# Optimization experiments

Measured on AMD Instinct MI355X. Metric: run time of the kernel, lower is better.

The kernel has to match this reference:

```python
import jax, jax.numpy as jnp
import numpy as np

N_NODES = 100000
N_EDGES = 1600000
IN_DIM = 128
OUT_DIM = 128
LEAKY_SLOPE = 0.01  # torch nn.LeakyReLU default


def setup_inputs() -> dict:
    key = jax.random.key(0)
    k1, k2, k3, k4 = jax.random.split(key, 4)
    x = jax.random.normal(k1, (N_NODES, IN_DIM), dtype=jnp.float32)
    edge_index = jax.random.randint(k2, (2, N_EDGES), 0, N_NODES, dtype=jnp.int64)
    edge_attr = jax.random.uniform(k3, (N_EDGES,), dtype=jnp.float32)
    # Linear params (xavier_uniform weight, zero bias)
    limit = np.sqrt(6.0 / (IN_DIM + OUT_DIM)).astype(np.float32)
    W = jax.random.uniform(k4, (OUT_DIM, IN_DIM), minval=-limit, maxval=limit, dtype=jnp.float32)
    b = jnp.zeros((OUT_DIM,), dtype=jnp.float32)
    return {"x": x, "edge_index": edge_index, "edge_attr": edge_attr, "W": W, "b": b}


def reference(x, edge_index, edge_attr, W, b):
    src = edge_index[0]  # x_j (source nodes)
    dst = edge_index[1]  # aggregation index (target nodes)
    # message: gather source features, scale by per-edge scalar  [E, D]
    msg = x[src] * edge_attr[:, None]
    # aggregate: scatter-add over target index  [N, D]
    agg = jax.ops.segment_sum(msg, dst, num_segments=N_NODES)
    # update: Linear + LeakyReLU (dropout is identity at p=0 / eval)
    out = agg @ W.T + b
    return jnp.where(out >= 0, out, LEAKY_SLOPE * out)
```

## Files before the change

kernel.cpp:

```cpp
#include <hip/hip_runtime.h>

#define N_NODES 100000
#define N_EDGES 1600000
#define DIM 128
#define LEAKY 0.01f
#define RS_STRIDE 132
#define WS_STRIDE 132
#define NBUCKET 391
#define SB_EDGES 4096
#define NSB 391

typedef short bf16x8 __attribute__((ext_vector_type(8)));
typedef float f32x4 __attribute__((ext_vector_type(4)));

static __device__ __forceinline__ unsigned short f2bf(float f) {
  unsigned int u = __float_as_uint(f);
  u = (u + 0x7fffu + ((u >> 16) & 1u)) >> 16;
  return (unsigned short)u;
}

__global__ __launch_bounds__(512) void sort_local_kernel(
    const int* __restrict__ ei, const float* __restrict__ attr,
    int2* __restrict__ binned, unsigned short* __restrict__ counts,
    int* __restrict__ srcOff) {
  __shared__ int hist[NBUCKET];
  __shared__ int cursor[NBUCKET];
  __shared__ int scanBuf[512];
  __shared__ int2 stage[SB_EDGES];

  const int t = threadIdx.x;
  const int blk = blockIdx.x;
  const int base = blk * SB_EDGES;
  const int n = min(SB_EDGES, N_EDGES - base);

  if (t < NBUCKET) hist[t] = 0;
  __syncthreads();

  int myP[8];
  int myB[8];
  float myA[8];
#pragma unroll
  for (int k = 0; k < 8; ++k) {
    int i = t + k * 512;
    if (i < n) {
      int e = base + i;
      int s = ei[e];
      int d = ei[N_EDGES + e];
      myA[k] = attr[e];
      myB[k] = d >> 8;
      myP[k] = s | ((d & 255) << 17);
      atomicAdd(&hist[myB[k]], 1);
    } else {
      myB[k] = -1;
    }
  }
  __syncthreads();

  int v = (t < NBUCKET) ? hist[t] : 0;
  scanBuf[t] = v;
  __syncthreads();
  for (int off = 1; off < 512; off <<= 1) {
    int u = (t >= off) ? scanBuf[t - off] : 0;
    __syncthreads();
    scanBuf[t] += u;
    __syncthreads();
  }
  if (t < NBUCKET) {
    int excl = scanBuf[t] - v;
    cursor[t] = excl;
    counts[(size_t)t * NSB + blk] = (unsigned short)v;
    srcOff[(size_t)t * NSB + blk] = base + excl;
  }
  __syncthreads();

#pragma unroll
  for (int k = 0; k < 8; ++k) {
    if (myB[k] >= 0) {
      int loc = atomicAdd(&cursor[myB[k]], 1);
      stage[loc] = make_int2(myP[k], __float_as_int(myA[k]));
    }
  }
  __syncthreads();

  for (int i = t; i < n; i += 512) binned[base + i] = stage[i];
}

__global__ __launch_bounds__(128) void bucket_count_kernel(
    const unsigned short* __restrict__ counts, int* __restrict__ bucketCount) {
  __shared__ int red[128];
  const int b = blockIdx.x;
  const int t = threadIdx.x;
  int s = 0;
  for (int sb = t; sb < NSB; sb += 128) s += counts[(size_t)b * NSB + sb];
  red[t] = s;
  __syncthreads();
  for (int off = 64; off > 0; off >>= 1) {
    if (t < off) red[t] += red[t + off];
    __syncthreads();
  }
  if (t == 0) bucketCount[b] = red[0];
}

__global__ __launch_bounds__(512) void bucket_scan_kernel(
    const int* __restrict__ bucketCount, int* __restrict__ bucketBase) {
  __shared__ int s[512];
  const int t = threadIdx.x;
  int v = (t < NBUCKET) ? bucketCount[t] : 0;
  s[t] = v;
  __syncthreads();
  for (int off = 1; off < 512; off <<= 1) {
    int u = (t >= off) ? s[t - off] : 0;
    __syncthreads();
    s[t] += u;
    __syncthreads();
  }
  if (t < NBUCKET) bucketBase[t] = s[t] - v;
}

__global__ __launch_bounds__(448) void passB_kernel(
    const int2* __restrict__ binned, const unsigned short* __restrict__ counts,
    const int* __restrict__ srcOff, const int* __restrict__ bucketBase,
    int2* __restrict__ csr, int* __restrict__ row_ptr) {
  __shared__ int runSrc[NSB];
  __shared__ int runLen[NSB];
  __shared__ int hist[256];
  __shared__ int cur[256];
  __shared__ int scanBuf[256];

  const int b = blockIdx.x;
  const int t = threadIdx.x;

  if (t < NSB) {
    runSrc[t] = srcOff[(size_t)b * NSB + t];
    runLen[t] = (int)counts[(size_t)b * NSB + t];
  }
  if (t < 256) hist[t] = 0;
  __syncthreads();

  if (t < NSB) {
    const int src = runSrc[t];
    const int len = runLen[t];
    for (int j = 0; j < len; ++j) {
      int px = binned[src + j].x;
      atomicAdd(&hist[(px >> 17) & 255], 1);
    }
  }
  __syncthreads();

  int hv = (t < 256) ? hist[t] : 0;
  if (t < 256) scanBuf[t] = hv;
  __syncthreads();
  for (int off = 1; off < 256; off <<= 1) {
    int u = 0;
    if (t < 256 && t >= off) u = scanBuf[t - off];
    __syncthreads();
    if (t < 256) scanBuf[t] += u;
    __syncthreads();
  }
  const int bb = bucketBase[b];
  if (t < 256) {
    int excl = scanBuf[t] - hv;
    cur[t] = excl;
    int node = b * 256 + t;
    if (node < N_NODES) row_ptr[node] = bb + excl;
  }
  if (b == 0 && t == 0) row_ptr[N_NODES] = N_EDGES;
  __syncthreads();

  if (t < NSB) {
    const int src = runSrc[t];
    const int len = runLen[t];
    for (int j = 0; j < len; ++j) {
      int2 rec = binned[src + j];
      int ld = (rec.x >> 17) & 255;
      int pos = bb + atomicAdd(&cur[ld], 1);
      csr[pos] = make_int2(rec.x & 0x1FFFF, rec.y);
    }
  }
}

__global__ __launch_bounds__(256) void x2b_kernel(
    const float4* __restrict__ x, ushort4* __restrict__ xb) {
  const int i = blockIdx.x * 256 + threadIdx.x;
  float4 v = x[i];
  ushort4 o;
  o.x = f2bf(v.x); o.y = f2bf(v.y); o.z = f2bf(v.z); o.w = f2bf(v.w);
  xb[i] = o;
}

__global__ __launch_bounds__(256) void w_frag_kernel(
    const float* __restrict__ W, bf16x8* __restrict__ wfrag) {
  const int gid = blockIdx.x * 256 + threadIdx.x;
  const int lane = gid & 63;
  const int q = (gid >> 6) & 3;
  const int nt = gid >> 8;
  const int n = nt * 16 + (lane & 15);
  const int kb = q * 32 + ((lane >> 4) & 3) * 8;
  const float4 f0 = *(const float4*)(W + n * DIM + kb);
  const float4 f1 = *(const float4*)(W + n * DIM + kb + 4);
  bf16x8 frag;
  frag[0] = (short)f2bf(f0.x); frag[1] = (short)f2bf(f0.y);
  frag[2] = (short)f2bf(f0.z); frag[3] = (short)f2bf(f0.w);
  frag[4] = (short)f2bf(f1.x); frag[5] = (short)f2bf(f1.y);
  frag[6] = (short)f2bf(f1.z); frag[7] = (short)f2bf(f1.w);
  wfrag[gid] = frag;
}

__global__ __launch_bounds__(256) void gather_aggb_kernel(
    const unsigned short* __restrict__ xb, const int* __restrict__ row_ptr,
    const int2* __restrict__ csr, unsigned int* __restrict__ aggB) {
  const int w = threadIdx.x >> 6;
  const int lane = threadIdx.x & 63;
  const int nA = blockIdx.x * 8 + w * 2;
  const int nB = nA + 1;

  int a = row_ptr[nA];
  const int aEnd = row_ptr[nA + 1];
  int b = row_ptr[nB];
  const int bEnd = row_ptr[nB + 1];

  float2 accA = make_float2(0.f, 0.f);
  float2 accB = make_float2(0.f, 0.f);

  while (a + 5 < aEnd && b + 5 < bEnd) {
    int2 ea[6], eb[6];
#pragma unroll
    for (int k = 0; k < 6; ++k) {
      ea[k] = csr[a + k];
      eb[k] = csr[b + k];
    }
    unsigned int ua[6], ub[6];
#pragma unroll
    for (int k = 0; k < 6; ++k) {
      ua[k] = *(const unsigned int*)(xb + (size_t)ea[k].x * DIM + lane * 2);
      ub[k] = *(const unsigned int*)(xb + (size_t)eb[k].x * DIM + lane * 2);
    }
#pragma unroll
    for (int k = 0; k < 6; ++k) {
      float fa = __int_as_float(ea[k].y);
      float fb = __int_as_float(eb[k].y);
      accA.x += __uint_as_float(ua[k] << 16) * fa;
      accA.y += __uint_as_float(ua[k] & 0xffff0000u) * fa;
      accB.x += __uint_as_float(ub[k] << 16) * fb;
      accB.y += __uint_as_float(ub[k] & 0xffff0000u) * fb;
    }
    a += 6;
    b += 6;
  }

  for (; a + 3 < aEnd; a += 4) {
    int2 e[4];
#pragma unroll
    for (int k = 0; k < 4; ++k) e[k] = csr[a + k];
    unsigned int u[4];
#pragma unroll
    for (int k = 0; k < 4; ++k)
      u[k] = *(const unsigned int*)(xb + (size_t)e[k].x * DIM + lane * 2);
#pragma unroll
    for (int k = 0; k < 4; ++k) {
      float f = __int_as_float(e[k].y);
      accA.x += __uint_as_float(u[k] << 16) * f;
      accA.y += __uint_as_float(u[k] & 0xffff0000u) * f;
    }
  }
  for (; a < aEnd; ++a) {
    int2 e0 = csr[a];
    float f0 = __int_as_float(e0.y);
    unsigned int u0 = *(const unsigned int*)(xb + (size_t)e0.x * DIM + lane * 2);
    accA.x += __uint_as_float(u0 << 16) * f0;
    accA.y += __uint_as_float(u0 & 0xffff0000u) * f0;
  }

  for (; b + 3 < bEnd; b += 4) {
    int2 e[4];
#pragma unroll
    for (int k = 0; k < 4; ++k) e[k] = csr[b + k];
    unsigned int u[4];
#pragma unroll
    for (int k = 0; k < 4; ++k)
      u[k] = *(const unsigned int*)(xb + (size_t)e[k].x * DIM + lane * 2);
#pragma unroll
    for (int k = 0; k < 4; ++k) {
      float f = __int_as_float(e[k].y);
      accB.x += __uint_as_float(u[k] << 16) * f;
      accB.y += __uint_as_float(u[k] & 0xffff0000u) * f;
    }
  }
  for (; b < bEnd; ++b) {
    int2 e0 = csr[b];
    float f0 = __int_as_float(e0.y);
    unsigned int u0 = *(const unsigned int*)(xb + (size_t)e0.x * DIM + lane * 2);
    accB.x += __uint_as_float(u0 << 16) * f0;
    accB.y += __uint_as_float(u0 & 0xffff0000u) * f0;
  }

  aggB[(size_t)nA * 64 + lane] =
      (unsigned int)f2bf(accA.x) | ((unsigned int)f2bf(accA.y) << 16);
  aggB[(size_t)nB * 64 + lane] =
      (unsigned int)f2bf(accB.x) | ((unsigned int)f2bf(accB.y) << 16);
}

__global__ __launch_bounds__(256) void gather_bf16_kernel(
    const unsigned short* __restrict__ xb, const int* __restrict__ row_ptr,
    const int2* __restrict__ csr, float* __restrict__ out) {
  const int node = blockIdx.x * 4 + (threadIdx.x >> 6);
  const int lane = threadIdx.x & 63;

  const int beg = row_ptr[node];
  const int end = row_ptr[node + 1];

  float2 acc = make_float2(0.f, 0.f);
  int e = beg;
  for (; e + 3 < end; e += 4) {
    int2 e0 = csr[e];
    int2 e1 = csr[e + 1];
    int2 e2 = csr[e + 2];
    int2 e3 = csr[e + 3];
    unsigned int u0 = *(const unsigned int*)(xb + (size_t)e0.x * DIM + lane * 2);
    unsigned int u1 = *(const unsigned int*)(xb + (size_t)e1.x * DIM + lane * 2);
    unsigned int u2 = *(const unsigned int*)(xb + (size_t)e2.x * DIM + lane * 2);
    unsigned int u3 = *(const unsigned int*)(xb + (size_t)e3.x * DIM + lane * 2);
    float a0 = __int_as_float(e0.y), a1 = __int_as_float(e1.y);
    float a2 = __int_as_float(e2.y), a3 = __int_as_float(e3.y);
    acc.x += __uint_as_float(u0 << 16) * a0;
    acc.y += __uint_as_float(u0 & 0xffff0000u) * a0;
    acc.x += __uint_as_float(u1 << 16) * a1;
    acc.y += __uint_as_float(u1 & 0xffff0000u) * a1;
    acc.x += __uint_as_float(u2 << 16) * a2;
    acc.y += __uint_as_float(u2 & 0xffff0000u) * a2;
    acc.x += __uint_as_float(u3 << 16) * a3;
    acc.y += __uint_as_float(u3 & 0xffff0000u) * a3;
  }
  for (; e < end; ++e) {
    int2 e0 = csr[e];
    float a0 = __int_as_float(e0.y);
    unsigned int u0 = *(const unsigned int*)(xb + (size_t)e0.x * DIM + lane * 2);
    acc.x += __uint_as_float(u0 << 16) * a0;
    acc.y += __uint_as_float(u0 & 0xffff0000u) * a0;
  }
  *(float2*)(out + (size_t)node * DIM + lane * 2) = acc;
}

__global__ __launch_bounds__(256) void gather_f32_kernel(
    const float* __restrict__ x, const int* __restrict__ row_ptr,
    const int2* __restrict__ csr, float* __restrict__ out) {
  const int node = blockIdx.x * 4 + (threadIdx.x >> 6);
  const int lane = threadIdx.x & 63;

  const int beg = row_ptr[node];
  const int end = row_ptr[node + 1];

  float2 acc = make_float2(0.f, 0.f);
  int e = beg;
  for (; e + 3 < end; e += 4) {
    int2 e0 = csr[e];
    int2 e1 = csr[e + 1];
    int2 e2 = csr[e + 2];
    int2 e3 = csr[e + 3];
    float2 v0 = *(const float2*)(x + (size_t)e0.x * DIM + lane * 2);
    float2 v1 = *(const float2*)(x + (size_t)e1.x * DIM + lane * 2);
    float2 v2 = *(const float2*)(x + (size_t)e2.x * DIM + lane * 2);
    float2 v3 = *(const float2*)(x + (size_t)e3.x * DIM + lane * 2);
    float a0 = __int_as_float(e0.y), a1 = __int_as_float(e1.y);
    float a2 = __int_as_float(e2.y), a3 = __int_as_float(e3.y);
    acc.x += v0.x * a0; acc.y += v0.y * a0;
    acc.x += v1.x * a1; acc.y += v1.y * a1;
    acc.x += v2.x * a2; acc.y += v2.y * a2;
    acc.x += v3.x * a3; acc.y += v3.y * a3;
  }
  for (; e < end; ++e) {
    int2 e0 = csr[e];
    float a0 = __int_as_float(e0.y);
    float2 v0 = *(const float2*)(x + (size_t)e0.x * DIM + lane * 2);
    acc.x += v0.x * a0; acc.y += v0.y * a0;
  }
  *(float2*)(out + (size_t)node * DIM + lane * 2) = acc;
}

__global__ __launch_bounds__(256) void linear_mfma_bf16_kernel(
    const unsigned short* __restrict__ aggB, const bf16x8* __restrict__ wfrag,
    const float* __restrict__ bias, float* __restrict__ out) {
  const int wave = threadIdx.x >> 6;
  const int lane = threadIdx.x & 63;
  const int r0 = (blockIdx.x * 4 + wave) * 16;
  if (r0 >= N_NODES) return;

  const int m = lane & 15;
  const int quad = lane >> 4;
  const int row = r0 + m;

  bf16x8 afrag[4];
#pragma unroll
  for (int q = 0; q < 4; ++q) {
    afrag[q] = *(const bf16x8*)(aggB + (size_t)row * DIM + q * 32 + quad * 8);
  }

#pragma unroll
  for (int nt = 0; nt < 8; ++nt) {
    const float bv = bias[nt * 16 + m];
    f32x4 acc = {bv, bv, bv, bv};
#pragma unroll
    for (int q = 0; q < 4; ++q) {
      bf16x8 bfrag = wfrag[(nt * 4 + q) * 64 + lane];
      acc = __builtin_amdgcn_mfma_f32_16x16x32_bf16(afrag[q], bfrag, acc, 0, 0, 0);
    }
    const int col = nt * 16 + m;
#pragma unroll
    for (int i = 0; i < 4; ++i) {
      float v = acc[i];
      v = v >= 0.f ? v : v * LEAKY;
      out[(size_t)(r0 + quad * 4 + i) * DIM + col] = v;
    }
  }
}

__global__ __launch_bounds__(256) void linear_mfma_kernel(
    const float* __restrict__ agg, const bf16x8* __restrict__ wfrag,
    const float* __restrict__ bias, float* __restrict__ out) {
  const int wave = threadIdx.x >> 6;
  const int lane = threadIdx.x & 63;
  const int r0 = (blockIdx.x * 4 + wave) * 16;
  if (r0 >= N_NODES) return;

  const int m = lane & 15;
  const int quad = lane >> 4;
  const int row = r0 + m;

  bf16x8 afrag[4];
#pragma unroll
  for (int q = 0; q < 4; ++q) {
    const float* ap = agg + (size_t)row * DIM + q * 32 + quad * 8;
    const float4 f0 = *(const float4*)(ap);
    const float4 f1 = *(const float4*)(ap + 4);
    afrag[q][0] = (short)f2bf(f0.x); afrag[q][1] = (short)f2bf(f0.y);
    afrag[q][2] = (short)f2bf(f0.z); afrag[q][3] = (short)f2bf(f0.w);
    afrag[q][4] = (short)f2bf(f1.x); afrag[q][5] = (short)f2bf(f1.y);
    afrag[q][6] = (short)f2bf(f1.z); afrag[q][7] = (short)f2bf(f1.w);
  }

#pragma unroll
  for (int nt = 0; nt < 8; ++nt) {
    const float bv = bias[nt * 16 + m];
    f32x4 acc = {bv, bv, bv, bv};
#pragma unroll
    for (int q = 0; q < 4; ++q) {
      bf16x8 bfrag = wfrag[(nt * 4 + q) * 64 + lane];
      acc = __builtin_amdgcn_mfma_f32_16x16x32_bf16(afrag[q], bfrag, acc, 0, 0, 0);
    }
    const int col = nt * 16 + m;
#pragma unroll
    for (int i = 0; i < 4; ++i) {
      float v = acc[i];
      v = v >= 0.f ? v : v * LEAKY;
      out[(size_t)(r0 + quad * 4 + i) * DIM + col] = v;
    }
  }
}

__global__ __launch_bounds__(256) void scatter_kernel(
    const float* __restrict__ x, const int* __restrict__ ei,
    const float* __restrict__ attr, float* __restrict__ agg) {
  int gid = blockIdx.x * blockDim.x + threadIdx.x;
  int e = gid >> 5;
  int f = (gid & 31) * 4;
  if (e >= N_EDGES) return;
  int s = ei[e];
  int d = ei[N_EDGES + e];
  float a = attr[e];
  const float4 xv = *(const float4*)(x + (size_t)s * DIM + f);
  float* dp = agg + (size_t)d * DIM + f;
  atomicAdd(dp + 0, xv.x * a);
  atomicAdd(dp + 1, xv.y * a);
  atomicAdd(dp + 2, xv.z * a);
  atomicAdd(dp + 3, xv.w * a);
}

__global__ __launch_bounds__(256, 2) void linear_kernel(
    const float* __restrict__ agg, const float* __restrict__ W,
    const float* __restrict__ bias, float* __restrict__ out) {
  __shared__ float Rs[32 * RS_STRIDE];
  __shared__ float Ws[64 * WS_STRIDE];

  const int tid = threadIdx.x;
  const int c = (tid & 31) * 4;
  const int rg = tid >> 5;
  const size_t rowBase = (size_t)blockIdx.x * 32;

  {
    const int lr = tid >> 3;
    const int col = (tid & 7) * 16;
    const float4* src = (const float4*)(agg + (rowBase + lr) * DIM + col);
#pragma unroll
    for (int j = 0; j < 4; ++j) {
      *(float4*)(Rs + lr * RS_STRIDE + col + j * 4) = src[j];
    }
  }

  const float4 bv = *(const float4*)(bias + c);
  float4 acc0 = bv, acc1 = bv, acc2 = bv, acc3 = bv;

  for (int half = 0; half < 2; ++half) {
    __syncthreads();
    {
      const int k0 = tid >> 7;
      const int o = tid & 127;
#pragma unroll
      for (int kk = k0; kk < 64; kk += 2) {
        Ws[kk * WS_STRIDE + o] = W[o * DIM + half * 64 + kk];
      }
    }
    __syncthreads();

    const float* rs0 = Rs + (rg * 4 + 0) * RS_STRIDE + half * 64;
    const float* rs1 = Rs + (rg * 4 + 1) * RS_STRIDE + half * 64;
    const float* rs2 = Rs + (rg * 4 + 2) * RS_STRIDE + half * 64;
    const float* rs3 = Rs + (rg * 4 + 3) * RS_STRIDE + half * 64;

#pragma unroll 8
    for (int k4 = 0; k4 < 16; ++k4) {
      const float4 v0 = *(const float4*)(rs0 + k4 * 4);
      const float4 v1 = *(const float4*)(rs1 + k4 * 4);
      const float4 v2 = *(const float4*)(rs2 + k4 * 4);
      const float4 v3 = *(const float4*)(rs3 + k4 * 4);
      const float4 w0 = *(const float4*)(Ws + (k4 * 4 + 0) * WS_STRIDE + c);
      const float4 w1 = *(const float4*)(Ws + (k4 * 4 + 1) * WS_STRIDE + c);
      const float4 w2 = *(const float4*)(Ws + (k4 * 4 + 2) * WS_STRIDE + c);
      const float4 w3 = *(const float4*)(Ws + (k4 * 4 + 3) * WS_STRIDE + c);

#define FMA4(acc, v)                                               \
      acc.x += v.x * w0.x + v.y * w1.x + v.z * w2.x + v.w * w3.x;  \
      acc.y += v.x * w0.y + v.y * w1.y + v.z * w2.y + v.w * w3.y;  \
      acc.z += v.x * w0.z + v.y * w1.z + v.z * w2.z + v.w * w3.z;  \
      acc.w += v.x * w0.w + v.y * w1.w + v.z * w2.w + v.w * w3.w;
      FMA4(acc0, v0)
      FMA4(acc1, v1)
      FMA4(acc2, v2)
      FMA4(acc3, v3)
#undef FMA4
    }
  }

#define LEAKY4(acc)                                   \
  acc.x = acc.x >= 0.f ? acc.x : acc.x * LEAKY;       \
  acc.y = acc.y >= 0.f ? acc.y : acc.y * LEAKY;       \
  acc.z = acc.z >= 0.f ? acc.z : acc.z * LEAKY;       \
  acc.w = acc.w >= 0.f ? acc.w : acc.w * LEAKY;
  LEAKY4(acc0) LEAKY4(acc1) LEAKY4(acc2) LEAKY4(acc3)
#undef LEAKY4

  const int row0 = (int)rowBase + rg * 4;
  *(float4*)(out + (size_t)(row0 + 0) * DIM + c) = acc0;
  *(float4*)(out + (size_t)(row0 + 1) * DIM + c) = acc1;
  *(float4*)(out + (size_t)(row0 + 2) * DIM + c) = acc2;
  *(float4*)(out + (size_t)(row0 + 3) * DIM + c) = acc3;
}

extern "C" void kernel_launch(void* const* d_in, const int* in_sizes, int n_in,
                              void* d_out, int out_size, void* d_ws, size_t ws_size,
                              hipStream_t stream) {
  const float* x = (const float*)d_in[0];
  const int* ei = (const int*)d_in[1];
  const float* attr = (const float*)d_in[2];
  const float* W = (const float*)d_in[3];
  const float* b = (const float*)d_in[4];
  float* out = (float*)d_out;

  const size_t offBinned = 0;
  const size_t offCounts = 12812288;
  const size_t offSrcOff = offCounts + 305920;
  const size_t offBCount = offSrcOff + 611584;
  const size_t offBBase  = offBCount + 1792;
  const size_t offCsr    = offBBase + 1792;
  const size_t offRowPtr = offCsr + 12812288;
  const size_t offWfrag  = offRowPtr + 400128;
  const size_t sortNeed  = offWfrag + 32768;
  const size_t offXb     = sortNeed;
  const size_t fullNeed  = offXb + 25600000;
  const size_t offAggB   = fullNeed;
  const size_t bf16Need  = offAggB + 25600000;

  if (ws_size >= sortNeed) {
    char* ws = (char*)d_ws;
    int2* binned = (int2*)(ws + offBinned);
    unsigned short* counts = (unsigned short*)(ws + offCounts);
    int* srcOff = (int*)(ws + offSrcOff);
    int* bucketCount = (int*)(ws + offBCount);
    int* bucketBase = (int*)(ws + offBBase);
    int2* csr = (int2*)(ws + offCsr);
    int* row_ptr = (int*)(ws + offRowPtr);
    bf16x8* wfrag = (bf16x8*)(ws + offWfrag);
    const bool haveXb = ws_size >= fullNeed;
    const bool haveAggB = ws_size >= bf16Need;
    unsigned short* xb = haveXb ? (unsigned short*)(ws + offXb) : nullptr;
    unsigned int* aggB = haveAggB ? (unsigned int*)(ws + offAggB) : nullptr;

    w_frag_kernel<<<8, 256, 0, stream>>>(W, wfrag);
    sort_local_kernel<<<NSB, 512, 0, stream>>>(ei, attr, binned, counts, srcOff);
    bucket_count_kernel<<<NBUCKET, 128, 0, stream>>>(counts, bucketCount);
    bucket_scan_kernel<<<1, 512, 0, stream>>>(bucketCount, bucketBase);
    passB_kernel<<<NBUCKET, 448, 0, stream>>>(binned, counts, srcOff, bucketBase,
                                              csr, row_ptr);
    if (haveAggB) {
      x2b_kernel<<<12500, 256, 0, stream>>>((const float4*)x, (ushort4*)xb);
      gather_aggb_kernel<<<N_NODES / 8, 256, 0, stream>>>(xb, row_ptr, csr, aggB);
      linear_mfma_bf16_kernel<<<(N_NODES + 63) / 64, 256, 0, stream>>>(
          (const unsigned short*)aggB, wfrag, b, out);
    } else if (haveXb) {
      x2b_kernel<<<12500, 256, 0, stream>>>((const float4*)x, (ushort4*)xb);
      gather_bf16_kernel<<<N_NODES / 4, 256, 0, stream>>>(xb, row_ptr, csr, out);
      linear_mfma_kernel<<<(N_NODES + 63) / 64, 256, 0, stream>>>(out, wfrag, b, out);
    } else {
      gather_f32_kernel<<<N_NODES / 4, 256, 0, stream>>>(x, row_ptr, csr, out);
      linear_mfma_kernel<<<(N_NODES + 63) / 64, 256, 0, stream>>>(out, wfrag, b, out);
    }
  } else {
    hipMemsetAsync(out, 0, (size_t)N_NODES * DIM * sizeof(float), stream);
    scatter_kernel<<<(N_EDGES * 32) / 256, 256, 0, stream>>>(x, ei, attr, out);
    linear_kernel<<<N_NODES / 32, 256, 0, stream>>>(out, W, b, out);
  }
}
```

Measured before the change: 240.3 us.

## Compute per-node degrees with global atomics and drop the histogram pass

The sort kernel now counts each destination node's in-degree with global atomics. A two-level scan over those degrees builds row_ptr and the bucket bases directly. This removes the old first pass in passB that re-read every binned record to build a local histogram. The placement kernel unrolls its record reads four at a time for more memory-level parallelism. The cost is 1.6M global atomics, an extra memset and an extra small kernel launch.

```diff
diff --git a/kernel.cpp b/kernel.cpp
--- a/kernel.cpp
+++ b/kernel.cpp
@@ -22,7 +22,7 @@
 __global__ __launch_bounds__(512) void sort_local_kernel(
     const int* __restrict__ ei, const float* __restrict__ attr,
     int2* __restrict__ binned, unsigned short* __restrict__ counts,
-    int* __restrict__ srcOff) {
+    int* __restrict__ srcOff, int* __restrict__ deg) {
   __shared__ int hist[NBUCKET];
   __shared__ int cursor[NBUCKET];
   __shared__ int scanBuf[512];
@@ -50,6 +50,7 @@
       myB[k] = d >> 8;
       myP[k] = s | ((d & 255) << 17);
       atomicAdd(&hist[myB[k]], 1);
+      atomicAdd(&deg[d], 1);
     } else {
       myB[k] = -1;
     }
@@ -85,20 +86,24 @@
   for (int i = t; i < n; i += 512) binned[base + i] = stage[i];
 }
 
-__global__ __launch_bounds__(128) void bucket_count_kernel(
-    const unsigned short* __restrict__ counts, int* __restrict__ bucketCount) {
-  __shared__ int red[128];
+__global__ __launch_bounds__(256) void scanA_kernel(
+    const int* __restrict__ deg, int* __restrict__ row_ptr,
+    int* __restrict__ bucketCount) {
+  __shared__ int s[256];
   const int b = blockIdx.x;
   const int t = threadIdx.x;
-  int s = 0;
-  for (int sb = t; sb < NSB; sb += 128) s += counts[(size_t)b * NSB + sb];
-  red[t] = s;
-  __syncthreads();
-  for (int off = 64; off > 0; off >>= 1) {
-    if (t < off) red[t] += red[t + off];
-    __syncthreads();
-  }
-  if (t == 0) bucketCount[b] = red[0];
+  const int node = b * 256 + t;
+  const int v = (node < N_NODES) ? deg[node] : 0;
+  s[t] = v;
+  __syncthreads();
+  for (int off = 1; off < 256; off <<= 1) {
+    int u = (t >= off) ? s[t - off] : 0;
+    __syncthreads();
+    s[t] += u;
+    __syncthreads();
+  }
+  if (node < N_NODES) row_ptr[node] = s[t] - v;
+  if (t == 0) bucketCount[b] = s[255];
 }
 
 __global__ __launch_bounds__(512) void bucket_scan_kernel(
@@ -117,15 +122,22 @@
   if (t < NBUCKET) bucketBase[t] = s[t] - v;
 }
 
-__global__ __launch_bounds__(448) void passB_kernel(
+__global__ __launch_bounds__(256) void scanB_kernel(
+    int* __restrict__ row_ptr, const int* __restrict__ bucketBase) {
+  const int b = blockIdx.x;
+  const int t = threadIdx.x;
+  const int node = b * 256 + t;
+  if (node < N_NODES) row_ptr[node] += bucketBase[b];
+  if (b == 0 && t == 0) row_ptr[N_NODES] = N_EDGES;
+}
+
+__global__ __launch_bounds__(448) void place_kernel(
     const int2* __restrict__ binned, const unsigned short* __restrict__ counts,
-    const int* __restrict__ srcOff, const int* __restrict__ bucketBase,
-    int2* __restrict__ csr, int* __restrict__ row_ptr) {
+    const int* __restrict__ srcOff, const int* __restrict__ row_ptr,
+    int2* __restrict__ csr) {
   __shared__ int runSrc[NSB];
   __shared__ int runLen[NSB];
-  __shared__ int hist[256];
   __shared__ int cur[256];
-  __shared__ int scanBuf[256];
 
   const int b = blockIdx.x;
   const int t = threadIdx.x;
@@ -134,47 +146,34 @@
     runSrc[t] = srcOff[(size_t)b * NSB + t];
     runLen[t] = (int)counts[(size_t)b * NSB + t];
   }
-  if (t < 256) hist[t] = 0;
+  if (t < 256) {
+    const int node = b * 256 + t;
+    cur[t] = (node < N_NODES) ? row_ptr[node] : 0;
+  }
   __syncthreads();
 
   if (t < NSB) {
     const int src = runSrc[t];
     const int len = runLen[t];
-    for (int j = 0; j < len; ++j) {
-      int px = binned[src + j].x;
-      atomicAdd(&hist[(px >> 17) & 255], 1);
-    }
-  }
-  __syncthreads();
-
-  int hv = (t < 256) ? hist[t] : 0;
-  if (t < 256) scanBuf[t] = hv;
-  __syncthreads();
-  for (int off = 1; off < 256; off <<= 1) {
-    int u = 0;
-    if (t < 256 && t >= off) u = scanBuf[t - off];
-    __syncthreads();
-    if (t < 256) scanBuf[t] += u;
-    __syncthreads();
-  }
-  const int bb = bucketBase[b];
-  if (t < 256) {
-    int excl = scanBuf[t] - hv;
-    cur[t] = excl;
-    int node = b * 256 + t;
-    if (node < N_NODES) row_ptr[node] = bb + excl;
-  }
-  if (b == 0 && t == 0) row_ptr[N_NODES] = N_EDGES;
-  __syncthreads();
-
-  if (t < NSB) {
-    const int src = runSrc[t];
-    const int len = runLen[t];
-    for (int j = 0; j < len; ++j) {
-      int2 rec = binned[src + j];
-      int ld = (rec.x >> 17) & 255;
-      int pos = bb + atomicAdd(&cur[ld], 1);
-      csr[pos] = make_int2(rec.x & 0x1FFFF, rec.y);
+    int j = 0;
+    for (; j + 3 < len; j += 4) {
+      int2 r0 = binned[src + j];
+      int2 r1 = binned[src + j + 1];
+      int2 r2 = binned[src + j + 2];
+      int2 r3 = binned[src + j + 3];
+      int p0 = atomicAdd(&cur[(r0.x >> 17) & 255], 1);
+      int p1 = atomicAdd(&cur[(r1.x >> 17) & 255], 1);
+      int p2 = atomicAdd(&cur[(r2.x >> 17) & 255], 1);
+      int p3 = atomicAdd(&cur[(r3.x >> 17) & 255], 1);
+      csr[p0] = make_int2(r0.x & 0x1FFFF, r0.y);
+      csr[p1] = make_int2(r1.x & 0x1FFFF, r1.y);
+      csr[p2] = make_int2(r2.x & 0x1FFFF, r2.y);
+      csr[p3] = make_int2(r3.x & 0x1FFFF, r3.y);
+    }
+    for (; j < len; ++j) {
+      int2 r0 = binned[src + j];
+      int p0 = atomicAdd(&cur[(r0.x >> 17) & 255], 1);
+      csr[p0] = make_int2(r0.x & 0x1FFFF, r0.y);
     }
   }
 }
@@ -568,7 +567,8 @@
   const size_t offBinned = 0;
   const size_t offCounts = 12812288;
   const size_t offSrcOff = offCounts + 305920;
-  const size_t offBCount = offSrcOff + 611584;
+  const size_t offDeg    = offSrcOff + 611584;
+  const size_t offBCount = offDeg + 400128;
   const size_t offBBase  = offBCount + 1792;
   const size_t offCsr    = offBBase + 1792;
   const size_t offRowPtr = offCsr + 12812288;
@@ -584,6 +584,7 @@
     int2* binned = (int2*)(ws + offBinned);
     unsigned short* counts = (unsigned short*)(ws + offCounts);
     int* srcOff = (int*)(ws + offSrcOff);
+    int* deg = (int*)(ws + offDeg);
     int* bucketCount = (int*)(ws + offBCount);
     int* bucketBase = (int*)(ws + offBBase);
     int2* csr = (int2*)(ws + offCsr);
@@ -594,12 +595,15 @@
     unsigned short* xb = haveXb ? (unsigned short*)(ws + offXb) : nullptr;
     unsigned int* aggB = haveAggB ? (unsigned int*)(ws + offAggB) : nullptr;
 
+    hipMemsetAsync(deg, 0, (size_t)N_NODES * sizeof(int), stream);
     w_frag_kernel<<<8, 256, 0, stream>>>(W, wfrag);
-    sort_local_kernel<<<NSB, 512, 0, stream>>>(ei, attr, binned, counts, srcOff);
-    bucket_count_kernel<<<NBUCKET, 128, 0, stream>>>(counts, bucketCount);
+    sort_local_kernel<<<NSB, 512, 0, stream>>>(ei, attr, binned, counts, srcOff,
+                                               deg);
+    scanA_kernel<<<NBUCKET, 256, 0, stream>>>(deg, row_ptr, bucketCount);
     bucket_scan_kernel<<<1, 512, 0, stream>>>(bucketCount, bucketBase);
-    passB_kernel<<<NBUCKET, 448, 0, stream>>>(binned, counts, srcOff, bucketBase,
-                                              csr, row_ptr);
+    scanB_kernel<<<NBUCKET, 256, 0, stream>>>(row_ptr, bucketBase);
+    place_kernel<<<NBUCKET, 448, 0, stream>>>(binned, counts, srcOff, row_ptr,
+                                              csr);
     if (haveAggB) {
       x2b_kernel<<<12500, 256, 0, stream>>>((const float4*)x, (ushort4*)xb);
       gather_aggb_kernel<<<N_NODES / 8, 256, 0, stream>>>(xb, row_ptr, csr, aggB);
```

After: 290.5 us. 1.21x slower.

## Halve sort superblock size and process two runs per thread in passB

Applied to the files above, without the earlier changes.

Shrinks each sort superblock from 4096 to 2048 edges, doubling the number of sort_local blocks so the local binning sees more parallelism and uses less shared staging per block. Source offsets are stored as 16-bit local offsets, with the superblock base rebuilt in passB, so the metadata takes no more space even with twice as many runs. In passB each thread now walks two runs in interleaved fashion to keep more independent loads in flight. The cost is twice as many short runs per bucket, more loop overhead, and a less even per-thread work split.

```diff
diff --git a/kernel.cpp b/kernel.cpp
--- a/kernel.cpp
+++ b/kernel.cpp
@@ -7,8 +7,8 @@
 #define RS_STRIDE 132
 #define WS_STRIDE 132
 #define NBUCKET 391
-#define SB_EDGES 4096
-#define NSB 391
+#define SB_EDGES 2048
+#define NSB 782
 
 typedef short bf16x8 __attribute__((ext_vector_type(8)));
 typedef float f32x4 __attribute__((ext_vector_type(4)));
@@ -22,7 +22,7 @@
 __global__ __launch_bounds__(512) void sort_local_kernel(
     const int* __restrict__ ei, const float* __restrict__ attr,
     int2* __restrict__ binned, unsigned short* __restrict__ counts,
-    int* __restrict__ srcOff) {
+    unsigned short* __restrict__ srcOffU) {
   __shared__ int hist[NBUCKET];
   __shared__ int cursor[NBUCKET];
   __shared__ int scanBuf[512];
@@ -36,11 +36,11 @@
   if (t < NBUCKET) hist[t] = 0;
   __syncthreads();
 
-  int myP[8];
-  int myB[8];
-  float myA[8];
-#pragma unroll
-  for (int k = 0; k < 8; ++k) {
+  int myP[4];
+  int myB[4];
+  float myA[4];
+#pragma unroll
+  for (int k = 0; k < 4; ++k) {
     int i = t + k * 512;
     if (i < n) {
       int e = base + i;
@@ -69,12 +69,12 @@
     int excl = scanBuf[t] - v;
     cursor[t] = excl;
     counts[(size_t)t * NSB + blk] = (unsigned short)v;
-    srcOff[(size_t)t * NSB + blk] = base + excl;
-  }
-  __syncthreads();
-
-#pragma unroll
-  for (int k = 0; k < 8; ++k) {
+    srcOffU[(size_t)t * NSB + blk] = (unsigned short)excl;
+  }
+  __syncthreads();
+
+#pragma unroll
+  for (int k = 0; k < 4; ++k) {
     if (myB[k] >= 0) {
       int loc = atomicAdd(&cursor[myB[k]], 1);
       stage[loc] = make_int2(myP[k], __float_as_int(myA[k]));
@@ -119,8 +119,9 @@
 
 __global__ __launch_bounds__(448) void passB_kernel(
     const int2* __restrict__ binned, const unsigned short* __restrict__ counts,
-    const int* __restrict__ srcOff, const int* __restrict__ bucketBase,
-    int2* __restrict__ csr, int* __restrict__ row_ptr) {
+    const unsigned short* __restrict__ srcOffU,
+    const int* __restrict__ bucketBase, int2* __restrict__ csr,
+    int* __restrict__ row_ptr) {
   __shared__ int runSrc[NSB];
   __shared__ int runLen[NSB];
   __shared__ int hist[256];
@@ -130,20 +131,26 @@
   const int b = blockIdx.x;
   const int t = threadIdx.x;
 
-  if (t < NSB) {
-    runSrc[t] = srcOff[(size_t)b * NSB + t];
-    runLen[t] = (int)counts[(size_t)b * NSB + t];
+  for (int idx = t; idx < NSB; idx += 448) {
+    runSrc[idx] = idx * SB_EDGES + (int)srcOffU[(size_t)b * NSB + idx];
+    runLen[idx] = (int)counts[(size_t)b * NSB + idx];
   }
   if (t < 256) hist[t] = 0;
   __syncthreads();
 
-  if (t < NSB) {
-    const int src = runSrc[t];
-    const int len = runLen[t];
-    for (int j = 0; j < len; ++j) {
-      int px = binned[src + j].x;
-      atomicAdd(&hist[(px >> 17) & 255], 1);
-    }
+  if (t < NBUCKET) {
+    const int sA = runSrc[t], lA = runLen[t];
+    const int sB = runSrc[t + NBUCKET], lB = runLen[t + NBUCKET];
+    int ja = 0, jb = 0;
+    while (ja < lA && jb < lB) {
+      int pxA = binned[sA + ja].x;
+      int pxB = binned[sB + jb].x;
+      atomicAdd(&hist[(pxA >> 17) & 255], 1);
+      atomicAdd(&hist[(pxB >> 17) & 255], 1);
+      ++ja; ++jb;
+    }
+    for (; ja < lA; ++ja) atomicAdd(&hist[(binned[sA + ja].x >> 17) & 255], 1);
+    for (; jb < lB; ++jb) atomicAdd(&hist[(binned[sB + jb].x >> 17) & 255], 1);
   }
   __syncthreads();
 
@@ -167,14 +174,28 @@
   if (b == 0 && t == 0) row_ptr[N_NODES] = N_EDGES;
   __syncthreads();
 
-  if (t < NSB) {
-    const int src = runSrc[t];
-    const int len = runLen[t];
-    for (int j = 0; j < len; ++j) {
-      int2 rec = binned[src + j];
-      int ld = (rec.x >> 17) & 255;
-      int pos = bb + atomicAdd(&cur[ld], 1);
-      csr[pos] = make_int2(rec.x & 0x1FFFF, rec.y);
+  if (t < NBUCKET) {
+    const int sA = runSrc[t], lA = runLen[t];
+    const int sB = runSrc[t + NBUCKET], lB = runLen[t + NBUCKET];
+    int ja = 0, jb = 0;
+    while (ja < lA && jb < lB) {
+      int2 rA = binned[sA + ja];
+      int2 rB = binned[sB + jb];
+      int pA = bb + atomicAdd(&cur[(rA.x >> 17) & 255], 1);
+      int pB = bb + atomicAdd(&cur[(rB.x >> 17) & 255], 1);
+      csr[pA] = make_int2(rA.x & 0x1FFFF, rA.y);
+      csr[pB] = make_int2(rB.x & 0x1FFFF, rB.y);
+      ++ja; ++jb;
+    }
+    for (; ja < lA; ++ja) {
+      int2 r = binned[sA + ja];
+      int p = bb + atomicAdd(&cur[(r.x >> 17) & 255], 1);
+      csr[p] = make_int2(r.x & 0x1FFFF, r.y);
+    }
+    for (; jb < lB; ++jb) {
+      int2 r = binned[sB + jb];
+      int p = bb + atomicAdd(&cur[(r.x >> 17) & 255], 1);
+      csr[p] = make_int2(r.x & 0x1FFFF, r.y);
     }
   }
 }
@@ -566,12 +587,12 @@
   float* out = (float*)d_out;
 
   const size_t offBinned = 0;
-  const size_t offCounts = 12812288;
-  const size_t offSrcOff = offCounts + 305920;
+  const size_t offCounts = 12800000;
+  const size_t offSrcOff = offCounts + 611584;
   const size_t offBCount = offSrcOff + 611584;
   const size_t offBBase  = offBCount + 1792;
   const size_t offCsr    = offBBase + 1792;
-  const size_t offRowPtr = offCsr + 12812288;
+  const size_t offRowPtr = offCsr + 12800000;
   const size_t offWfrag  = offRowPtr + 400128;
   const size_t sortNeed  = offWfrag + 32768;
   const size_t offXb     = sortNeed;
@@ -583,7 +604,7 @@
     char* ws = (char*)d_ws;
     int2* binned = (int2*)(ws + offBinned);
     unsigned short* counts = (unsigned short*)(ws + offCounts);
-    int* srcOff = (int*)(ws + offSrcOff);
+    unsigned short* srcOffU = (unsigned short*)(ws + offSrcOff);
     int* bucketCount = (int*)(ws + offBCount);
     int* bucketBase = (int*)(ws + offBBase);
     int2* csr = (int2*)(ws + offCsr);
@@ -595,10 +616,10 @@
     unsigned int* aggB = haveAggB ? (unsigned int*)(ws + offAggB) : nullptr;
 
     w_frag_kernel<<<8, 256, 0, stream>>>(W, wfrag);
-    sort_local_kernel<<<NSB, 512, 0, stream>>>(ei, attr, binned, counts, srcOff);
+    sort_local_kernel<<<NSB, 512, 0, stream>>>(ei, attr, binned, counts, srcOffU);
     bucket_count_kernel<<<NBUCKET, 128, 0, stream>>>(counts, bucketCount);
     bucket_scan_kernel<<<1, 512, 0, stream>>>(bucketCount, bucketBase);
-    passB_kernel<<<NBUCKET, 448, 0, stream>>>(binned, counts, srcOff, bucketBase,
+    passB_kernel<<<NBUCKET, 448, 0, stream>>>(binned, counts, srcOffU, bucketBase,
                                               csr, row_ptr);
     if (haveAggB) {
       x2b_kernel<<<12500, 256, 0, stream>>>((const float4*)x, (ushort4*)xb);
```

New measurement: 246.7 us. 2.7% more time.
